# Optimization experiments

Hardware: AMD Instinct MI355X
Metric: run time of the kernel (lower is better)

## Reference

```python
import jax, jax.numpy as jnp
import numpy as np

N = 50000      # nodes
E = 800000     # edges (avg degree 16)
IN = 128       # in_channels
H = 256        # hidden_channels
EPS = 1e-5     # BatchNorm eps


def setup_inputs() -> dict:
    key = jax.random.key(0)
    ks = iter(jax.random.split(key, 40))
    nrm = lambda shape, s: jax.random.normal(next(ks), shape, dtype=jnp.float32) * s
    d = {}
    d["x"] = nrm((N, IN), 1.0)
    d["edge_index"] = jax.random.randint(next(ks), (2, E), 0, N, dtype=jnp.int32)
    # SAGEConv layers: lin_l (neighbors, with bias) + lin_r (root, no bias); BatchNorm params
    dims = [(IN, H), (H, H), (H, H)]
    for i, (fi, fo) in enumerate(dims):
        s = 1.0 / np.sqrt(fi)
        d[f"w_l{i}"] = nrm((fo, fi), s)
        d[f"b_l{i}"] = nrm((fo,), s)
        d[f"w_r{i}"] = nrm((fo, fi), s)
        d[f"g{i}"] = jnp.ones((fo,), jnp.float32)
        d[f"be{i}"] = nrm((fo,), 0.1)
        d[f"rm{i}"] = nrm((fo,), 0.1)
        d[f"rv{i}"] = jax.random.uniform(next(ks), (fo,), jnp.float32, 0.5, 1.5)
    # predictor MLP: H->H, H->H//2, H//2->1
    for j, (fi, fo) in enumerate([(H, H), (H, H // 2), (H // 2, 1)], start=1):
        s = 1.0 / np.sqrt(fi)
        d[f"pw{j}"] = nrm((fo, fi), s)
        d[f"pb{j}"] = nrm((fo,), s)
    return d


def _sage(x, src, dst, w_l, b_l, w_r):
    # mean aggregation of neighbor messages (gather by src, scatter-add by dst)
    msum = jax.ops.segment_sum(x[src], dst, num_segments=N)       # [N, F]
    cnt = jax.ops.segment_sum(jnp.ones((src.shape[0], 1), x.dtype), dst, num_segments=N)
    mean = msum / jnp.maximum(cnt, 1.0)
    return mean @ w_l.T + b_l + x @ w_r.T


def _bn(x, g, be, rm, rv):
    return (x - rm) * jax.lax.rsqrt(rv + EPS) * g + be


def reference(x, edge_index,
              w_l0, b_l0, w_r0, g0, be0, rm0, rv0,
              w_l1, b_l1, w_r1, g1, be1, rm1, rv1,
              w_l2, b_l2, w_r2, g2, be2, rm2, rv2,
              pw1, pb1, pw2, pb2, pw3, pb3):
    src, dst = edge_index[0], edge_index[1]
    layers = [
        (w_l0, b_l0, w_r0, g0, be0, rm0, rv0),
        (w_l1, b_l1, w_r1, g1, be1, rm1, rv1),
        (w_l2, b_l2, w_r2, g2, be2, rm2, rv2),
    ]
    for (wl, bl, wr, g, be, rm, rv) in layers:
        x = _sage(x, src, dst, wl, bl, wr)
        x = jax.nn.relu(_bn(x, g, be, rm, rv))
        # dropout: identity in eval mode
    h = jax.nn.relu(x @ pw1.T + pb1)
    h = jax.nn.relu(h @ pw2.T + pb2)
    return jax.nn.sigmoid(h @ pw3.T + pb3)   # [N, 1]
```

## Files before the change

### kernel.cpp

```cpp
#include <hip/hip_runtime.h>
#include <hip/hip_fp16.h>

#define NNODES 50000
#define NEDGES 800000

typedef _Float16 f16;
typedef f16 f16x8 __attribute__((ext_vector_type(8)));
typedef f16 f16x4 __attribute__((ext_vector_type(4)));
typedef float f32x4 __attribute__((ext_vector_type(4)));

#define GLOAD_LDS16(g, l) __builtin_amdgcn_global_load_lds( \
    (const __attribute__((address_space(1))) void*)(g), \
    (__attribute__((address_space(3))) void*)(l), 16, 0, 0)


__global__ void k_bsum(const int* __restrict__ deg, int* __restrict__ bsum, int n) {
    __shared__ int s[256];
    int i = blockIdx.x * 256 + threadIdx.x;
    s[threadIdx.x] = (i < n) ? ((deg[i] + 7) & ~7) : 0;
    __syncthreads();
    for (int off = 128; off; off >>= 1) {
        if (threadIdx.x < off) s[threadIdx.x] += s[threadIdx.x + off];
        __syncthreads();
    }
    if (threadIdx.x == 0) bsum[blockIdx.x] = s[0];
}

__global__ void k_scan_bsum(int* __restrict__ bsum, int nb) {
    int lane = threadIdx.x & 63;
    int carry = 0;
    for (int base = 0; base < nb; base += 64) {
        int i = base + lane;
        int v = (i < nb) ? bsum[i] : 0;
        int orig = v;
        for (int off = 1; off < 64; off <<= 1) {
            int x = __shfl_up(v, off);
            if (lane >= off) v += x;
        }
        if (i < nb) bsum[i] = carry + v - orig;
        carry += __shfl(v, 63);
    }
}

__global__ void k_offsets(const int* __restrict__ deg, const int* __restrict__ bsum,
                          int* __restrict__ offs, int n) {
    __shared__ int s[256];
    int t = threadIdx.x;
    int i = blockIdx.x * 256 + t;
    int v = (i < n) ? ((deg[i] + 7) & ~7) : 0;
    s[t] = v;
    __syncthreads();
    for (int off = 1; off < 256; off <<= 1) {
        int x = (t >= off) ? s[t - off] : 0;
        __syncthreads();
        s[t] += x;
        __syncthreads();
    }
    if (i < n) offs[i] = bsum[blockIdx.x] + s[t] - v;
    if (i == n - 1) offs[n] = bsum[blockIdx.x] + s[t];
}

__global__ void k_scatter_pad(const int* __restrict__ src, const int* __restrict__ dst,
                              const int* __restrict__ offs, const int* __restrict__ deg,
                              int* __restrict__ cursor, int* __restrict__ csr,
                              int E, int n) {
    int tid = blockIdx.x * blockDim.x + threadIdx.x;
    int nthr = gridDim.x * blockDim.x;
    int d[4], s[4], ob[4], p[4];
    bool ok[4];
#pragma unroll
    for (int u = 0; u < 4; ++u) {
        int e = tid + u * nthr;
        ok[u] = (e < E);
        d[u] = ok[u] ? dst[e] : 0;
        s[u] = ok[u] ? src[e] : 0;
    }
#pragma unroll
    for (int u = 0; u < 4; ++u) ob[u] = ok[u] ? offs[d[u]] : 0;
#pragma unroll
    for (int u = 0; u < 4; ++u) p[u] = ok[u] ? atomicAdd(&cursor[d[u]], 1) : 0;
#pragma unroll
    for (int u = 0; u < 4; ++u) if (ok[u]) csr[ob[u] + p[u]] = s[u];
    for (int v = tid; v < n; v += nthr) {
        int dd = deg[v], pd = (dd + 7) & ~7;
        int base = offs[v];
        for (int q = dd; q < pd; ++q) csr[base + q] = NNODES;
    }
}


#define NPK 8
struct PackSeg { const float* w; f16* p; int FO; int K; };
struct AffSeg { const float *b, *g, *be, *rm, *rv; float *cs, *cb; int n; int isbn; };

struct FrontArgs {
    const int* dst; int* deg;
    const float* x; f16* h0; int n4;
    const float* pw3; f16* pw3f;
    f16 *hA, *hB;
    PackSeg ps[NPK];
    AffSeg as[5];
};

__global__ void k_front(FrontArgs a) {
    int b = blockIdx.x, tid = threadIdx.x;
    if (b < 1024) {
        int t = b * 256 + tid, stride = 1024 * 256;
        int dd[4]; bool ok[4];
#pragma unroll
        for (int u = 0; u < 4; ++u) {
            int e = t + u * stride;
            ok[u] = (e < NEDGES);
            dd[u] = ok[u] ? a.dst[e] : 0;
        }
#pragma unroll
        for (int u = 0; u < 4; ++u) if (ok[u]) atomicAdd(&a.deg[dd[u]], 1);
    } else if (b < 2624) {
        int i = (b - 1024) * 256 + tid, stride = 1600 * 256;
        for (; i < a.n4; i += stride) {
            float4 v = ((const float4*)a.x)[i];
            f16x4 o;
            o[0] = (f16)v.x; o[1] = (f16)v.y; o[2] = (f16)v.z; o[3] = (f16)v.w;
            ((f16x4*)a.h0)[i] = o;
        }
    } else if (b < 2880) {
        int gid = (b - 2624) * 256 + tid, gstride = 256 * 256;
        for (int sgi = 0; sgi < NPK; ++sgi) {
            PackSeg sg = a.ps[sgi];
            int total = sg.FO * sg.K / 8;
            int KS = sg.K >> 5;
            for (int t2 = gid; t2 < total; t2 += gstride) {
                int lane = t2 & 63;
                int tile = t2 >> 6;
                int ks = tile % KS, nt = tile / KS;
                int row = nt * 16 + (lane & 15);
                int col = ks * 32 + (lane >> 4) * 8;
                const float4* srcp = (const float4*)(sg.w + (size_t)row * sg.K + col);
                float4 v0 = srcp[0], v1 = srcp[1];
                f16x8 o;
                o[0] = (f16)v0.x; o[1] = (f16)v0.y; o[2] = (f16)v0.z; o[3] = (f16)v0.w;
                o[4] = (f16)v1.x; o[5] = (f16)v1.y; o[6] = (f16)v1.z; o[7] = (f16)v1.w;
                ((f16x8*)sg.p)[t2] = o;
            }
        }
    } else if (b < 2885) {
        AffSeg sg = a.as[b - 2880];
        if (tid < sg.n) {
            if (sg.isbn) {
                float sc = sg.g[tid] * rsqrtf(sg.rv[tid] + 1e-5f);
                sg.cs[tid] = sc;
                sg.cb[tid] = (sg.b[tid] - sg.rm[tid]) * sc + sg.be[tid];
            } else {
                sg.cs[tid] = 1.0f;
                sg.cb[tid] = sg.b[tid];
            }
        }
    } else {
        f16x4 z = {};
        if (tid < 32) {
            ((f16x4*)(a.h0 + (size_t)NNODES * 128))[tid] = z;
        } else if (tid < 96) {
            ((f16x4*)(a.hA + (size_t)NNODES * 256))[tid - 32] = z;
        } else if (tid < 160) {
            ((f16x4*)(a.hB + (size_t)NNODES * 256))[tid - 96] = z;
        } else if (tid < 192) {
            int i = tid - 160;
            float4 v = ((const float4*)a.pw3)[i];
            f16x4 o;
            o[0] = (f16)v.x; o[1] = (f16)v.y; o[2] = (f16)v.z; o[3] = (f16)v.w;
            ((f16x4*)a.pw3f)[i] = o;
        }
    }
}

template <int F>
__global__ __launch_bounds__(256) void k_aggregate(
    const f16* __restrict__ h, const int* __restrict__ poffs,
    const int* __restrict__ deg, const int* __restrict__ csr,
    f16* __restrict__ mean) {
    constexpr int LPN = F / 8;
    constexpr int NPW = 64 / LPN;
    int tid = threadIdx.x;
    int wave = tid >> 6, lane = tid & 63;
    int node = blockIdx.x * (4 * NPW) + wave * NPW + lane / LPN;
    int t = lane % LPN;
    int beg = poffs[node], end = poffs[node + 1];
    int nb = (end - beg) >> 3;
    const f16x8* hb = (const f16x8*)h;
    float acc[8] = {0.f, 0.f, 0.f, 0.f, 0.f, 0.f, 0.f, 0.f};

    int j = beg;
    for (int p = 0; p + 2 <= nb; p += 2, j += 16) {
        int iA[8], iB[8];
#pragma unroll
        for (int u = 0; u < 8; ++u) iA[u] = csr[j + u];
#pragma unroll
        for (int u = 0; u < 8; ++u) iB[u] = csr[j + 8 + u];
        f16x8 vA[8], vB[8];
#pragma unroll
        for (int u = 0; u < 8; ++u) vA[u] = hb[(size_t)iA[u] * LPN + t];
#pragma unroll
        for (int u = 0; u < 8; ++u) vB[u] = hb[(size_t)iB[u] * LPN + t];
#pragma unroll
        for (int u = 0; u < 8; ++u)
#pragma unroll
            for (int e = 0; e < 8; ++e) acc[e] += (float)vA[u][e];
#pragma unroll
        for (int u = 0; u < 8; ++u)
#pragma unroll
            for (int e = 0; e < 8; ++e) acc[e] += (float)vB[u][e];
    }
    if (nb & 1) {
        int iA[8];
#pragma unroll
        for (int u = 0; u < 8; ++u) iA[u] = csr[j + u];
        f16x8 vA[8];
#pragma unroll
        for (int u = 0; u < 8; ++u) vA[u] = hb[(size_t)iA[u] * LPN + t];
#pragma unroll
        for (int u = 0; u < 8; ++u)
#pragma unroll
            for (int e = 0; e < 8; ++e) acc[e] += (float)vA[u][e];
    }

    int d = deg[node];
    float inv = (d > 0) ? 1.0f / (float)d : 0.0f;
    f16x8 o;
#pragma unroll
    for (int e = 0; e < 8; ++e) o[e] = (f16)(acc[e] * inv);
    ((f16x8*)mean)[(size_t)node * LPN + t] = o;
}

template <int FO, bool FUSE>
__global__ __launch_bounds__(FO * 2, 4) void k_gemm(
    const f16* __restrict__ A1, const f16* __restrict__ A2,
    const f16* __restrict__ W1p, const f16* __restrict__ W2p,
    const float* __restrict__ cs, const float* __restrict__ cb,
    f16* __restrict__ out, const f16* __restrict__ w3,
    const float* __restrict__ pb3, float* __restrict__ outF,
    int M, int K) {
    constexpr int WC = FO / 64;
    constexpr int NT = FO * 2;
    __shared__ f16 As[2][128 * 64];
    __shared__ float smF[WC][128];
    int tid = threadIdx.x;
    int lane = tid & 63;
    int wave = tid >> 6;
    int wr = wave / WC, wc = wave % WC;
    int m0 = blockIdx.x * 128;
    int lrow = lane & 15;
    int kof8 = (lane >> 4) * 8;
    int KC1 = K >> 6;
    int KS = K >> 5;
    int NC = A2 ? KC1 * 2 : KC1;

    auto stage = [&](int buf, int c) {
        int ph = (c >= KC1) ? 1 : 0;
        const char* Ab = (const char*)(ph ? A2 : A1);
        int kb0 = ((c - ph * KC1) << 6) * 2;
        char* Al = (char*)&As[buf][0];
#pragma unroll
        for (int u0 = 0; u0 < 1024; u0 += NT) {
            int u = u0 + tid;
            int row = u >> 3;
            int kb = (u & 7) * 16;
            int grow = m0 + row; if (grow > M - 1) grow = M - 1;
            GLOAD_LDS16(Ab + (size_t)grow * (K * 2) + kb0 + (kb ^ ((row & 7) << 4)), Al + u * 16);
        }
    };

    f32x4 acc[4][4] = {};

    stage(0, 0);
    __syncthreads();

    for (int c = 0; c < NC; ++c) {
        int ph = (c >= KC1) ? 1 : 0;
        const f16x8* Wp = (const f16x8*)(ph ? W2p : W1p);
        int cl = c - ph * KC1;
        f16x8 b[2][4];
#pragma unroll
        for (int kk = 0; kk < 2; ++kk) {
            int ks = cl * 2 + kk;
#pragma unroll
            for (int ni = 0; ni < 4; ++ni) {
                int nt = wc * 4 + ni;
                b[kk][ni] = Wp[((size_t)nt * KS + ks) * 64 + lane];
            }
        }
        if (c + 1 < NC) stage((c + 1) & 1, c + 1);
        const char* Al = (const char*)&As[c & 1][0];
#pragma unroll
        for (int kk = 0; kk < 2; ++kk) {
            int kb = kof8 * 2 + kk * 64;
            f16x8 a[4];
#pragma unroll
            for (int mi = 0; mi < 4; ++mi) {
                int r = wr * 64 + mi * 16 + lrow;
                a[mi] = *(const f16x8*)(Al + r * 128 + (kb ^ ((r & 7) << 4)));
            }
#pragma unroll
            for (int mi = 0; mi < 4; ++mi)
#pragma unroll
                for (int ni = 0; ni < 4; ++ni)
                    acc[mi][ni] = __builtin_amdgcn_mfma_f32_16x16x32_f16(a[mi], b[kk][ni], acc[mi][ni], 0, 0, 0);
        }
        __syncthreads();
    }

    if constexpr (!FUSE) {
        int rquad = (lane >> 4) * 4;
#pragma unroll
        for (int mi = 0; mi < 4; ++mi) {
#pragma unroll
            for (int ni = 0; ni < 4; ++ni) {
                int col = wc * 64 + ni * 16 + (lane & 15);
                float s = cs[col], cc = cb[col];
#pragma unroll
                for (int r = 0; r < 4; ++r) {
                    int row = m0 + wr * 64 + mi * 16 + rquad + r;
                    if (row < M) {
                        float v = acc[mi][ni][r] * s + cc;
                        v = fmaxf(v, 0.f);
                        out[(size_t)row * FO + col] = (f16)v;
                    }
                }
            }
        }
    } else {
        float b3 = pb3[0];
        float rsum[4][4] = {};
#pragma unroll
        for (int ni = 0; ni < 4; ++ni) {
            int col = wc * 64 + ni * 16 + (lane & 15);
            float w3v = (float)w3[col];
            float cbv = cb[col];
#pragma unroll
            for (int mi = 0; mi < 4; ++mi)
#pragma unroll
                for (int r = 0; r < 4; ++r)
                    rsum[mi][r] += fmaxf(acc[mi][ni][r] + cbv, 0.f) * w3v;
        }
#pragma unroll
        for (int mi = 0; mi < 4; ++mi)
#pragma unroll
            for (int r = 0; r < 4; ++r) {
                float s = rsum[mi][r];
                s += __shfl_xor(s, 1); s += __shfl_xor(s, 2);
                s += __shfl_xor(s, 4); s += __shfl_xor(s, 8);
                if ((lane & 15) == 0)
                    smF[wc][wr * 64 + mi * 16 + (lane >> 4) * 4 + r] = s;
            }
        __syncthreads();
        if (tid < 128) {
            int row = m0 + tid;
            if (row < M) {
                float s = b3;
#pragma unroll
                for (int w = 0; w < WC; ++w) s += smF[w][tid];
                outF[row] = 1.0f / (1.0f + expf(-s));
            }
        }
    }
}


extern "C" void kernel_launch(void* const* d_in, const int* in_sizes, int n_in,
                              void* d_out, int out_size, void* d_ws, size_t ws_size,
                              hipStream_t stream) {
    const float* x = (const float*)d_in[0];
    const int* ei = (const int*)d_in[1];
    const int* src = ei;
    const int* dst = ei + NEDGES;
    const float* w_l[3] = {(const float*)d_in[2], (const float*)d_in[9], (const float*)d_in[16]};
    const float* b_l[3] = {(const float*)d_in[3], (const float*)d_in[10], (const float*)d_in[17]};
    const float* w_r[3] = {(const float*)d_in[4], (const float*)d_in[11], (const float*)d_in[18]};
    const float* g[3]  = {(const float*)d_in[5], (const float*)d_in[12], (const float*)d_in[19]};
    const float* be[3] = {(const float*)d_in[6], (const float*)d_in[13], (const float*)d_in[20]};
    const float* rm[3] = {(const float*)d_in[7], (const float*)d_in[14], (const float*)d_in[21]};
    const float* rv[3] = {(const float*)d_in[8], (const float*)d_in[15], (const float*)d_in[22]};
    const float* pw1 = (const float*)d_in[23]; const float* pb1 = (const float*)d_in[24];
    const float* pw2 = (const float*)d_in[25]; const float* pb2 = (const float*)d_in[26];
    const float* pw3 = (const float*)d_in[27]; const float* pb3 = (const float*)d_in[28];

    char* wsb = (char*)d_ws;
    size_t o = 0;
    auto alloc = [&](size_t b) { size_t r = o; o = (o + b + 255) & ~(size_t)255; return r; };

    size_t deg_off = alloc(NNODES * 4);
    size_t cur_off = alloc(NNODES * 4);
    int* deg    = (int*)(wsb + deg_off);
    int* cursor = (int*)(wsb + cur_off);
    int* poffs  = (int*)(wsb + alloc((NNODES + 1) * 4));
    int* bsum   = (int*)(wsb + alloc(256 * 4));
    int* csr    = (int*)(wsb + alloc((NEDGES + 8 * NNODES) * 4));
    f16* h0   = (f16*)(wsb + alloc((size_t)(NNODES + 1) * 128 * 2));
    f16* hA   = (f16*)(wsb + alloc((size_t)(NNODES + 1) * 256 * 2));
    f16* hB   = (f16*)(wsb + alloc((size_t)(NNODES + 1) * 256 * 2));
    f16* mean = (f16*)(wsb + alloc((size_t)NNODES * 256 * 2));
    f16* wl0p = (f16*)(wsb + alloc(256 * 128 * 2));
    f16* wr0p = (f16*)(wsb + alloc(256 * 128 * 2));
    f16* wl1p = (f16*)(wsb + alloc(256 * 256 * 2));
    f16* wr1p = (f16*)(wsb + alloc(256 * 256 * 2));
    f16* wl2p = (f16*)(wsb + alloc(256 * 256 * 2));
    f16* wr2p = (f16*)(wsb + alloc(256 * 256 * 2));
    f16* pw1p = (f16*)(wsb + alloc(256 * 256 * 2));
    f16* pw2p = (f16*)(wsb + alloc(128 * 256 * 2));
    f16* pw3f = (f16*)(wsb + alloc(128 * 2));
    float* csv[5]; float* cbv[5];
    for (int i = 0; i < 5; ++i) {
        csv[i] = (float*)(wsb + alloc(256 * 4));
        cbv[i] = (float*)(wsb + alloc(256 * 4));
    }

    hipMemsetAsync(wsb + deg_off, 0, cur_off - deg_off + NNODES * 4, stream);
    FrontArgs fa;
    fa.dst = dst; fa.deg = deg;
    fa.x = x; fa.h0 = h0; fa.n4 = NNODES * 128 / 4;
    fa.pw3 = pw3; fa.pw3f = pw3f;
    fa.hA = hA; fa.hB = hB;
    fa.ps[0] = {w_l[0], wl0p, 256, 128};
    fa.ps[1] = {w_r[0], wr0p, 256, 128};
    fa.ps[2] = {w_l[1], wl1p, 256, 256};
    fa.ps[3] = {w_r[1], wr1p, 256, 256};
    fa.ps[4] = {w_l[2], wl2p, 256, 256};
    fa.ps[5] = {w_r[2], wr2p, 256, 256};
    fa.ps[6] = {pw1,    pw1p, 256, 256};
    fa.ps[7] = {pw2,    pw2p, 128, 256};
    for (int i = 0; i < 3; ++i)
        fa.as[i] = {b_l[i], g[i], be[i], rm[i], rv[i], csv[i], cbv[i], 256, 1};
    fa.as[3] = {pb1, nullptr, nullptr, nullptr, nullptr, csv[3], cbv[3], 256, 0};
    fa.as[4] = {pb2, nullptr, nullptr, nullptr, nullptr, csv[4], cbv[4], 128, 0};
    k_front<<<2886, 256, 0, stream>>>(fa);

    int nb = (NNODES + 255) / 256;
    k_bsum<<<nb, 256, 0, stream>>>(deg, bsum, NNODES);
    k_scan_bsum<<<1, 64, 0, stream>>>(bsum, nb);
    k_offsets<<<nb, 256, 0, stream>>>(deg, bsum, poffs, NNODES);
    int gsc = (NEDGES / 4 + 255) / 256;
    k_scatter_pad<<<gsc, 256, 0, stream>>>(src, dst, poffs, deg, cursor, csr, NEDGES, NNODES);

    int gm = (NNODES + 127) / 128;

    k_aggregate<128><<<3125, 256, 0, stream>>>(h0, poffs, deg, csr, mean);
    k_gemm<256, false><<<gm, 512, 0, stream>>>(mean, h0, wl0p, wr0p, csv[0], cbv[0], hA,
                                               nullptr, nullptr, nullptr, NNODES, 128);
    k_aggregate<256><<<6250, 256, 0, stream>>>(hA, poffs, deg, csr, mean);
    k_gemm<256, false><<<gm, 512, 0, stream>>>(mean, hA, wl1p, wr1p, csv[1], cbv[1], hB,
                                               nullptr, nullptr, nullptr, NNODES, 256);
    k_aggregate<256><<<6250, 256, 0, stream>>>(hB, poffs, deg, csr, mean);
    k_gemm<256, false><<<gm, 512, 0, stream>>>(mean, hB, wl2p, wr2p, csv[2], cbv[2], hA,
                                               nullptr, nullptr, nullptr, NNODES, 256);
    k_gemm<256, false><<<gm, 512, 0, stream>>>(hA, nullptr, pw1p, nullptr, csv[3], cbv[3], hB,
                                               nullptr, nullptr, nullptr, NNODES, 256);
    k_gemm<128, true><<<gm, 256, 0, stream>>>(hB, nullptr, pw2p, nullptr, csv[4], cbv[4], nullptr,
                                              pw3f, pb3, (float*)d_out, NNODES, 256);
}
```

Measured before the change: 334.0 us.

## Split neighbor aggregation into feature slices across blocks for cache locality

The aggregation kernel now assigns each block a feature slice of 32 halves for 64 nodes, with 4 lanes per node, instead of processing whole feature rows. Consecutive blocks cover different slices of the same node chunk, so each gathered row segment is 64 bytes and the working set per slice is smaller, which is meant to improve L2 reuse of gathered rows. The trade-off is more blocks and CSR index reads repeated once per slice. Node indices past the end are clamped, so tail threads redundantly rewrite the last node.

```diff
diff --git a/kernel.cpp b/kernel.cpp
--- a/kernel.cpp
+++ b/kernel.cpp
@@ -173,17 +173,22 @@
     }
 }
 
-template <int F>
-__global__ __launch_bounds__(256) void k_aggregate(
+template <int F, int LOGS>
+__global__ __launch_bounds__(256) void k_aggx(
     const f16* __restrict__ h, const int* __restrict__ poffs,
     const int* __restrict__ deg, const int* __restrict__ csr,
     f16* __restrict__ mean) {
-    constexpr int LPN = F / 8;
-    constexpr int NPW = 64 / LPN;
+    constexpr int NS = 1 << LOGS;
+    constexpr int RS = F / 8;
+    int slice = blockIdx.x & (NS - 1);
+    int chunk = blockIdx.x >> LOGS;
     int tid = threadIdx.x;
     int wave = tid >> 6, lane = tid & 63;
-    int node = blockIdx.x * (4 * NPW) + wave * NPW + lane / LPN;
-    int t = lane % LPN;
+    int node = chunk * 64 + wave * 16 + (lane >> 2);
+    if (node > NNODES - 1) node = NNODES - 1;
+    int t = lane & 3;
+    int fbase = slice * 4 + t;
+
     int beg = poffs[node], end = poffs[node + 1];
     int nb = (end - beg) >> 3;
     const f16x8* hb = (const f16x8*)h;
@@ -198,9 +203,9 @@
         for (int u = 0; u < 8; ++u) iB[u] = csr[j + 8 + u];
         f16x8 vA[8], vB[8];
 #pragma unroll
-        for (int u = 0; u < 8; ++u) vA[u] = hb[(size_t)iA[u] * LPN + t];
-#pragma unroll
-        for (int u = 0; u < 8; ++u) vB[u] = hb[(size_t)iB[u] * LPN + t];
+        for (int u = 0; u < 8; ++u) vA[u] = hb[(size_t)iA[u] * RS + fbase];
+#pragma unroll
+        for (int u = 0; u < 8; ++u) vB[u] = hb[(size_t)iB[u] * RS + fbase];
 #pragma unroll
         for (int u = 0; u < 8; ++u)
 #pragma unroll
@@ -216,7 +221,7 @@
         for (int u = 0; u < 8; ++u) iA[u] = csr[j + u];
         f16x8 vA[8];
 #pragma unroll
-        for (int u = 0; u < 8; ++u) vA[u] = hb[(size_t)iA[u] * LPN + t];
+        for (int u = 0; u < 8; ++u) vA[u] = hb[(size_t)iA[u] * RS + fbase];
 #pragma unroll
         for (int u = 0; u < 8; ++u)
 #pragma unroll
@@ -228,7 +233,7 @@
     f16x8 o;
 #pragma unroll
     for (int e = 0; e < 8; ++e) o[e] = (f16)(acc[e] * inv);
-    ((f16x8*)mean)[(size_t)node * LPN + t] = o;
+    ((f16x8*)mean)[(size_t)node * RS + fbase] = o;
 }
 
 template <int FO, bool FUSE>
@@ -441,14 +446,15 @@
     k_scatter_pad<<<gsc, 256, 0, stream>>>(src, dst, poffs, deg, cursor, csr, NEDGES, NNODES);
 
     int gm = (NNODES + 127) / 128;
-
-    k_aggregate<128><<<3125, 256, 0, stream>>>(h0, poffs, deg, csr, mean);
+    int gch = (NNODES + 63) / 64;
+
+    k_aggx<128, 2><<<gch * 4, 256, 0, stream>>>(h0, poffs, deg, csr, mean);
     k_gemm<256, false><<<gm, 512, 0, stream>>>(mean, h0, wl0p, wr0p, csv[0], cbv[0], hA,
                                                nullptr, nullptr, nullptr, NNODES, 128);
-    k_aggregate<256><<<6250, 256, 0, stream>>>(hA, poffs, deg, csr, mean);
+    k_aggx<256, 3><<<gch * 8, 256, 0, stream>>>(hA, poffs, deg, csr, mean);
     k_gemm<256, false><<<gm, 512, 0, stream>>>(mean, hA, wl1p, wr1p, csv[1], cbv[1], hB,
                                                nullptr, nullptr, nullptr, NNODES, 256);
-    k_aggregate<256><<<6250, 256, 0, stream>>>(hB, poffs, deg, csr, mean);
+    k_aggx<256, 3><<<gch * 8, 256, 0, stream>>>(hB, poffs, deg, csr, mean);
     k_gemm<256, false><<<gm, 512, 0, stream>>>(mean, hB, wl2p, wr2p, csv[2], cbv[2], hA,
                                                nullptr, nullptr, nullptr, NNODES, 256);
     k_gemm<256, false><<<gm, 512, 0, stream>>>(hA, nullptr, pw1p, nullptr, csv[3], cbv[3], hB,
```

Result: slower. 376.0 us (+12.6%).
